# Performance work log

Measured on AMD Instinct MI355X. Metric: run time of the kernel, lower is better.

## Reference

```python
import jax, jax.numpy as jnp
import numpy as np

BATCH = 4096
FEAT = 1024
HID = 1024


def setup_inputs() -> dict:
    key = jax.random.key(0)
    ks = jax.random.split(key, 11)
    s_x = 1.0 / np.sqrt(FEAT)
    s_h = 1.0 / np.sqrt(HID)
    return {
        "x": jax.random.normal(ks[0], (BATCH, FEAT), jnp.float32),
        "h_prev": jax.random.normal(ks[1], (BATCH, HID), jnp.float32),
        "c_prev": jax.random.normal(ks[2], (BATCH, HID), jnp.float32),
        # Dense(3*hidden) on x and h (keras Dense: y = x @ W + b)
        "W_ifo_x": jax.random.normal(ks[3], (FEAT, 3 * HID), jnp.float32) * s_x,
        "b_ifo_x": jnp.zeros((3 * HID,), jnp.float32),
        "W_ifo_h": jax.random.normal(ks[4], (HID, 3 * HID), jnp.float32) * s_h,
        "b_ifo_h": jnp.zeros((3 * HID,), jnp.float32),
        # Dense(hidden) on x and h for candidate 'a'
        "W_b_x": jax.random.normal(ks[5], (FEAT, HID), jnp.float32) * s_x,
        "b_b_x": jnp.zeros((HID,), jnp.float32),
        "W_b_h": jax.random.normal(ks[6], (HID, HID), jnp.float32) * s_h,
        "b_b_h": jnp.zeros((HID,), jnp.float32),
    }


def reference(x, h_prev, c_prev, W_ifo_x, b_ifo_x, W_ifo_h, b_ifo_h,
              W_b_x, b_b_x, W_b_h, b_b_h):
    # Fused gate projections: [B, 3H]
    ifo = jax.nn.sigmoid(x @ W_ifo_x + b_ifo_x + h_prev @ W_ifo_h + b_ifo_h)
    i, f, o = jnp.split(ifo, 3, axis=-1)
    a = jnp.tanh(x @ W_b_x + b_b_x + h_prev @ W_b_h + b_b_h)
    c = i * a + f * c_prev
    h = o * jnp.tanh(c)
    return (h, c)
```

## Files before the change

### kernel.cpp

```cpp
#include <hip/hip_runtime.h>
#include <hip/hip_bf16.h>
#include <stdint.h>
#include <stddef.h>


#define BATCH 4096
#define FEAT  1024
#define HID   1024
#define NCAT  4096
#define KCAT  2048

typedef __attribute__((ext_vector_type(8))) __bf16 bf16x8;
typedef __attribute__((ext_vector_type(4))) float  floatx4;

__device__ __forceinline__ unsigned short f2bf(float f) {
    __hip_bfloat16 b = __float2bfloat16(f);
    return *reinterpret_cast<unsigned short*>(&b);
}
__device__ __forceinline__ void gl2lds16(const unsigned short* g, unsigned short* l) {
    __builtin_amdgcn_global_load_lds(
        (const __attribute__((address_space(1))) void*)g,
        (__attribute__((address_space(3))) void*)l, 16, 0, 0);
}

#define TP_PAD 72
__global__ __launch_bounds__(256)
void pack_all(const float* __restrict__ x, const float* __restrict__ h,
              const float* __restrict__ Wix, const float* __restrict__ Wih,
              const float* __restrict__ Wbx, const float* __restrict__ Wbh,
              unsigned short* __restrict__ Xcat, unsigned short* __restrict__ Wt) {
    __shared__ unsigned short tile[64 * TP_PAD];
    const int t = threadIdx.x;
    const int b = blockIdx.x;
    if (b >= 2048) {
        const int mbase = (b - 2048) * 4;
#pragma unroll
        for (int r = 0; r < 4; ++r) {
            const int m = mbase + r;
            const float* src = (t < 128) ? (x + (size_t)m * FEAT + t * 8)
                                         : (h + (size_t)m * HID + (t - 128) * 8);
            float4 v0 = *(const float4*)src;
            float4 v1 = *(const float4*)(src + 4);
            union { unsigned short s16[8]; uint4 v; } pk;
            pk.s16[0] = f2bf(v0.x); pk.s16[1] = f2bf(v0.y);
            pk.s16[2] = f2bf(v0.z); pk.s16[3] = f2bf(v0.w);
            pk.s16[4] = f2bf(v1.x); pk.s16[5] = f2bf(v1.y);
            pk.s16[6] = f2bf(v1.z); pk.s16[7] = f2bf(v1.w);
            *(uint4*)(Xcat + (size_t)m * KCAT + t * 8) = pk.v;
        }
        return;
    }
    const int tid = b;
    const int k0  = (tid & 31) * 64;
    const int q0  = (tid >> 5) * 64;
    const float* src; int stride, cb;
    if (q0 < 3072) { src = (k0 < FEAT) ? Wix : Wih; stride = 3072; cb = q0; }
    else           { src = (k0 < FEAT) ? Wbx : Wbh; stride = 1024; cb = q0 - 3072; }
    const int krow = (k0 < FEAT) ? k0 : (k0 - FEAT);
    {
        int kl = t >> 2;
        int c0 = (t & 3) * 16;
        const float* s = src + (size_t)(krow + kl) * stride + cb + c0;
        union { unsigned short s16[16]; uint4 v[2]; } tmp;
#pragma unroll
        for (int u = 0; u < 16; u += 4) {
            float4 v = *(const float4*)(s + u);
            tmp.s16[u + 0] = f2bf(v.x); tmp.s16[u + 1] = f2bf(v.y);
            tmp.s16[u + 2] = f2bf(v.z); tmp.s16[u + 3] = f2bf(v.w);
        }
        *(uint4*)&tile[kl * TP_PAD + c0]     = tmp.v[0];
        *(uint4*)&tile[kl * TP_PAD + c0 + 8] = tmp.v[1];
    }
    __syncthreads();
    {
        int nl = t >> 2, seg = t & 3;
        int q = q0 + nl;
        int g, j;
        if (q < 3072) { g = q >> 10; j = q & 1023; }
        else          { g = 3;       j = q - 3072; }
        int np = ((j >> 4) << 6) + (g << 4) + (j & 15);
        union { unsigned short s16[16]; uint4 v[2]; } pk;
#pragma unroll
        for (int u = 0; u < 16; ++u)
            pk.s16[u] = tile[(seg * 16 + u) * TP_PAD + nl];
        uint4* dst = (uint4*)(Wt + (size_t)np * KCAT + k0 + seg * 16);
        dst[0] = pk.v[0];
        dst[1] = pk.v[1];
    }
}

#define BM 256
#define BN 256
#define BK 64
#define NIT 16
#define HALF 8192

#define A_OFF(PAR, KS) (((PAR) * 2 + (KS)) * HALF)
#define B_OFF(PAR, KS) (32768 + ((PAR) * 2 + (KS)) * HALF)

__device__ __forceinline__ void stage_half(
    const unsigned short* __restrict__ src, int row0, int kt, int ks,
    unsigned short* __restrict__ ldsbase, int t) {
#pragma unroll
    for (int u = 0; u < 2; ++u) {
        int hslot = t + u * 512;
        int row   = hslot >> 2;
        int chofs = hslot & 3;
        int c     = chofs ^ ((row >> 1) & 3);
        gl2lds16(src + (size_t)(row0 + row) * KCAT + kt * BK + ks * 32 + c * 8,
                 ldsbase + hslot * 8);
    }
}

#define LOAD_BB(PAR, KS)                                                        \
    _Pragma("unroll")                                                           \
    for (int g = 0; g < 4; ++g)                                                 \
        bb[g] = *(const bf16x8*)&lds[B_OFF(PAR, KS) + (wn + g * 16 + lm) * 32 + cr];
#define LOAD_AA(PAR, KS, IQ)                                                    \
    _Pragma("unroll")                                                           \
    for (int ii = 0; ii < 4; ++ii)                                              \
        aa[ii] = *(const bf16x8*)&lds[A_OFF(PAR, KS) + (wm + (IQ) * 64 + ii * 16 + lm) * 32 + cr];
#define DO_MFMA(IQ)                                                             \
    asm volatile("s_waitcnt lgkmcnt(0)" ::: "memory");                          \
    __builtin_amdgcn_s_setprio(1);                                              \
    _Pragma("unroll")                                                           \
    for (int ii = 0; ii < 4; ++ii)                                              \
        _Pragma("unroll")                                                       \
        for (int g = 0; g < 4; ++g)                                             \
            acc[(IQ) * 4 + ii][g] = __builtin_amdgcn_mfma_f32_16x16x32_bf16(    \
                aa[ii], bb[g], acc[(IQ) * 4 + ii][g], 0, 0, 0);                 \
    __builtin_amdgcn_s_setprio(0);
#define BAR __builtin_amdgcn_s_barrier();

__global__ __launch_bounds__(512, 2)
void lstm_fused(const unsigned short* __restrict__ Xcat,
                const unsigned short* __restrict__ Wt,
                const float* __restrict__ c_prev,
                const float* __restrict__ bix, const float* __restrict__ bih,
                const float* __restrict__ bbx, const float* __restrict__ bbh,
                float* __restrict__ out_h, float* __restrict__ out_c) {
    __shared__ unsigned short lds[65536];
    const int t    = threadIdx.x;
    const int lane = t & 63;
    const int wid  = t >> 6;
    const int wm   = (wid >> 2) * 128;
    const int wn   = (wid & 3) * 64;
    const int m0   = blockIdx.y * BM;
    const int n0   = blockIdx.x * BN;
    const int lm   = lane & 15;
    const int lk   = lane >> 4;
    const int cr   = (lk ^ ((lm >> 1) & 3)) * 8;

    floatx4 acc[8][4];
#pragma unroll
    for (int i = 0; i < 8; ++i)
#pragma unroll
        for (int g = 0; g < 4; ++g) acc[i][g] = (floatx4){0.f, 0.f, 0.f, 0.f};

    stage_half(Xcat, m0, 0, 0, lds + A_OFF(0, 0), t);
    stage_half(Wt,   n0, 0, 0, lds + B_OFF(0, 0), t);
    stage_half(Xcat, m0, 0, 1, lds + A_OFF(0, 1), t);
    stage_half(Wt,   n0, 0, 1, lds + B_OFF(0, 1), t);
    stage_half(Xcat, m0, 1, 0, lds + A_OFF(1, 0), t);
    stage_half(Wt,   n0, 1, 0, lds + B_OFF(1, 0), t);
    asm volatile("s_waitcnt vmcnt(4)" ::: "memory");
    BAR

    bf16x8 aa[4], bb[4];

    for (int it = 0; it < NIT; ++it) {
        const int k1 = 2 * it + 1, k2 = 2 * it + 2, k3 = 2 * it + 3;
        const bool more = (it < NIT - 1);

        LOAD_BB(0, 0) LOAD_AA(0, 0, 0)
        stage_half(Xcat, m0, k1, 1, lds + A_OFF(1, 1), t);
        BAR DO_MFMA(0) BAR
        LOAD_AA(0, 0, 1)
        stage_half(Wt, n0, k1, 1, lds + B_OFF(1, 1), t);
        BAR DO_MFMA(1) BAR
        LOAD_BB(0, 1) LOAD_AA(0, 1, 0)
        if (more) stage_half(Xcat, m0, k2, 0, lds + A_OFF(0, 0), t);
        BAR DO_MFMA(0) BAR
        LOAD_AA(0, 1, 1)
        if (more) {
            stage_half(Wt, n0, k2, 0, lds + B_OFF(0, 0), t);
            asm volatile("s_waitcnt vmcnt(4)" ::: "memory");
        } else {
            asm volatile("s_waitcnt vmcnt(0)" ::: "memory");
        }
        BAR DO_MFMA(1) BAR
        LOAD_BB(1, 0) LOAD_AA(1, 0, 0)
        if (more) stage_half(Xcat, m0, k2, 1, lds + A_OFF(0, 1), t);
        BAR DO_MFMA(0) BAR
        LOAD_AA(1, 0, 1)
        if (more) stage_half(Wt, n0, k2, 1, lds + B_OFF(0, 1), t);
        BAR DO_MFMA(1) BAR
        LOAD_BB(1, 1) LOAD_AA(1, 1, 0)
        if (more) stage_half(Xcat, m0, k3, 0, lds + A_OFF(1, 0), t);
        BAR DO_MFMA(0) BAR
        LOAD_AA(1, 1, 1)
        if (more) {
            stage_half(Wt, n0, k3, 0, lds + B_OFF(1, 0), t);
            asm volatile("s_waitcnt vmcnt(4)" ::: "memory");
        }
        BAR DO_MFMA(1) BAR
    }

    const int j  = (((n0 + wn) >> 6) << 4) + lm;
    const float bi = bix[j]           + bih[j];
    const float bf = bix[HID + j]     + bih[HID + j];
    const float bo = bix[2 * HID + j] + bih[2 * HID + j];
    const float ba = bbx[j]           + bbh[j];
#pragma unroll
    for (int i = 0; i < 8; ++i) {
#pragma unroll
        for (int r = 0; r < 4; ++r) {
            int m = m0 + wm + i * 16 + (lk * 4) + r;
            float pi = acc[i][0][r] + bi;
            float pf = acc[i][1][r] + bf;
            float po = acc[i][2][r] + bo;
            float pa = acc[i][3][r] + ba;
            float ig = 1.f / (1.f + __expf(-pi));
            float fg = 1.f / (1.f + __expf(-pf));
            float og = 1.f / (1.f + __expf(-po));
            float av = 2.f / (1.f + __expf(-2.f * pa)) - 1.f;
            float cp = c_prev[(size_t)m * HID + j];
            float cv = ig * av + fg * cp;
            float hv = og * (2.f / (1.f + __expf(-2.f * cv)) - 1.f);
            out_h[(size_t)m * HID + j] = hv;
            out_c[(size_t)m * HID + j] = cv;
        }
    }
}

__global__ void naive_lstm(const float* __restrict__ x, const float* __restrict__ h,
                           const float* __restrict__ cvp,
                           const float* __restrict__ Wix, const float* __restrict__ bix,
                           const float* __restrict__ Wih, const float* __restrict__ bih,
                           const float* __restrict__ Wbx, const float* __restrict__ bbx,
                           const float* __restrict__ Wbh, const float* __restrict__ bbh,
                           float* __restrict__ out_h, float* __restrict__ out_c) {
    const int j = blockIdx.x * 256 + threadIdx.x;
    const int m = blockIdx.y;
    float ai = 0.f, af = 0.f, ao = 0.f, aa = 0.f;
    for (int k = 0; k < FEAT; ++k) {
        float xk = x[(size_t)m * FEAT + k];
        ai += xk * Wix[(size_t)k * 3072 + j];
        af += xk * Wix[(size_t)k * 3072 + HID + j];
        ao += xk * Wix[(size_t)k * 3072 + 2 * HID + j];
        aa += xk * Wbx[(size_t)k * HID + j];
    }
    for (int k = 0; k < HID; ++k) {
        float hk = h[(size_t)m * HID + k];
        ai += hk * Wih[(size_t)k * 3072 + j];
        af += hk * Wih[(size_t)k * 3072 + HID + j];
        ao += hk * Wih[(size_t)k * 3072 + 2 * HID + j];
        aa += hk * Wbh[(size_t)k * HID + j];
    }
    ai += bix[j] + bih[j];
    af += bix[HID + j] + bih[HID + j];
    ao += bix[2 * HID + j] + bih[2 * HID + j];
    aa += bbx[j] + bbh[j];
    float ig = 1.f / (1.f + __expf(-ai));
    float fg = 1.f / (1.f + __expf(-af));
    float og = 1.f / (1.f + __expf(-ao));
    float av = 2.f / (1.f + __expf(-2.f * aa)) - 1.f;
    float cp = cvp[(size_t)m * HID + j];
    float cc = ig * av + fg * cp;
    float hh = og * (2.f / (1.f + __expf(-2.f * cc)) - 1.f);
    out_h[(size_t)m * HID + j] = hh;
    out_c[(size_t)m * HID + j] = cc;
}

extern "C" void kernel_launch(void* const* d_in, const int* in_sizes, int n_in,
                              void* d_out, int out_size, void* d_ws, size_t ws_size,
                              hipStream_t stream) {
    const float* x   = (const float*)d_in[0];
    const float* h   = (const float*)d_in[1];
    const float* c   = (const float*)d_in[2];
    const float* Wix = (const float*)d_in[3];
    const float* bix = (const float*)d_in[4];
    const float* Wih = (const float*)d_in[5];
    const float* bih = (const float*)d_in[6];
    const float* Wbx = (const float*)d_in[7];
    const float* bbx = (const float*)d_in[8];
    const float* Wbh = (const float*)d_in[9];
    const float* bbh = (const float*)d_in[10];

    float* out_h = (float*)d_out;
    float* out_c = out_h + (size_t)BATCH * HID;

    const size_t WT_BYTES = (size_t)NCAT * KCAT * 2;
    const size_t XC_BYTES = (size_t)BATCH * KCAT * 2;
    if (ws_size >= WT_BYTES + XC_BYTES) {
        unsigned short* Wt   = (unsigned short*)d_ws;
        unsigned short* Xcat = (unsigned short*)((char*)d_ws + WT_BYTES);
        pack_all<<<2048 + 1024, 256, 0, stream>>>(x, h, Wix, Wih, Wbx, Wbh, Xcat, Wt);
        lstm_fused<<<dim3(NCAT / BN, BATCH / BM), 512, 0, stream>>>(
            Xcat, Wt, c, bix, bih, bbx, bbh, out_h, out_c);
    } else {
        naive_lstm<<<dim3(HID / 256, BATCH), 256, 0, stream>>>(
            x, h, c, Wix, bix, Wih, bih, Wbx, bbx, Wbh, bbh, out_h, out_c);
    }
}
```

Before: 200.2 us.

## Double-buffer A fragments in registers to overlap LDS reads with MFMA

Splits the A register fragments into two alternating buffers. The next quarter's A tile is read from LDS while the current quarter's MFMAs run, and the explicit lgkmcnt(0) wait before each MFMA group is dropped. Adds sched_barriers and reworks the vmcnt waits so staged data is ready in time. The cost it targets is LDS-read latency stalling the matrix cores. In exchange it uses more VGPRs, which may hurt occupancy at 2 blocks per CU. It also issues some LDS reads (such as the A_OFF(0,0) preload at the end of an iteration) before the workgroup barrier that publishes that tile, which risks reading data that is not yet visible.

```diff
diff --git a/kernel.cpp b/kernel.cpp
--- a/kernel.cpp
+++ b/kernel.cpp
@@ -112,25 +112,25 @@
     }
 }
 
-#define LOAD_BB(PAR, KS)                                                        \
+#define LOAD_B(PAR, KS)                                                         \
     _Pragma("unroll")                                                           \
     for (int g = 0; g < 4; ++g)                                                 \
         bb[g] = *(const bf16x8*)&lds[B_OFF(PAR, KS) + (wn + g * 16 + lm) * 32 + cr];
-#define LOAD_AA(PAR, KS, IQ)                                                    \
+#define LOAD_A(DST, PAR, KS, IQ)                                                \
     _Pragma("unroll")                                                           \
     for (int ii = 0; ii < 4; ++ii)                                              \
-        aa[ii] = *(const bf16x8*)&lds[A_OFF(PAR, KS) + (wm + (IQ) * 64 + ii * 16 + lm) * 32 + cr];
-#define DO_MFMA(IQ)                                                             \
-    asm volatile("s_waitcnt lgkmcnt(0)" ::: "memory");                          \
+        DST[ii] = *(const bf16x8*)&lds[A_OFF(PAR, KS) + (wm + (IQ) * 64 + ii * 16 + lm) * 32 + cr];
+#define MFMA_CL(SRC, IQ)                                                        \
     __builtin_amdgcn_s_setprio(1);                                              \
     _Pragma("unroll")                                                           \
     for (int ii = 0; ii < 4; ++ii)                                              \
         _Pragma("unroll")                                                       \
         for (int g = 0; g < 4; ++g)                                             \
             acc[(IQ) * 4 + ii][g] = __builtin_amdgcn_mfma_f32_16x16x32_bf16(    \
-                aa[ii], bb[g], acc[(IQ) * 4 + ii][g], 0, 0, 0);                 \
+                SRC[ii], bb[g], acc[(IQ) * 4 + ii][g], 0, 0, 0);                \
     __builtin_amdgcn_s_setprio(0);
 #define BAR __builtin_amdgcn_s_barrier();
+#define SBAR __builtin_amdgcn_sched_barrier(0);
 
 __global__ __launch_bounds__(512, 2)
 void lstm_fused(const unsigned short* __restrict__ Xcat,
@@ -166,44 +166,51 @@
     asm volatile("s_waitcnt vmcnt(4)" ::: "memory");
     BAR
 
-    bf16x8 aa[4], bb[4];
+    bf16x8 aaA[4], aaB[4], bb[4];
+    LOAD_A(aaA, 0, 0, 0)
 
     for (int it = 0; it < NIT; ++it) {
         const int k1 = 2 * it + 1, k2 = 2 * it + 2, k3 = 2 * it + 3;
         const bool more = (it < NIT - 1);
 
-        LOAD_BB(0, 0) LOAD_AA(0, 0, 0)
+        LOAD_B(0, 0) SBAR LOAD_A(aaB, 0, 0, 1)
         stage_half(Xcat, m0, k1, 1, lds + A_OFF(1, 1), t);
-        BAR DO_MFMA(0) BAR
-        LOAD_AA(0, 0, 1)
+        BAR MFMA_CL(aaA, 0) BAR
+        LOAD_A(aaA, 0, 1, 0)
         stage_half(Wt, n0, k1, 1, lds + B_OFF(1, 1), t);
-        BAR DO_MFMA(1) BAR
-        LOAD_BB(0, 1) LOAD_AA(0, 1, 0)
+        asm volatile("s_waitcnt vmcnt(4)" ::: "memory");
+        BAR MFMA_CL(aaB, 1) BAR
+        LOAD_B(0, 1) SBAR LOAD_A(aaB, 0, 1, 1)
         if (more) stage_half(Xcat, m0, k2, 0, lds + A_OFF(0, 0), t);
-        BAR DO_MFMA(0) BAR
-        LOAD_AA(0, 1, 1)
+        BAR MFMA_CL(aaA, 0) BAR
+        LOAD_A(aaA, 1, 0, 0)
         if (more) {
             stage_half(Wt, n0, k2, 0, lds + B_OFF(0, 0), t);
             asm volatile("s_waitcnt vmcnt(4)" ::: "memory");
         } else {
+            asm volatile("s_waitcnt vmcnt(2)" ::: "memory");
+        }
+        BAR MFMA_CL(aaB, 1) BAR
+        LOAD_B(1, 0) SBAR LOAD_A(aaB, 1, 0, 1)
+        if (more) stage_half(Xcat, m0, k2, 1, lds + A_OFF(0, 1), t);
+        BAR MFMA_CL(aaA, 0) BAR
+        LOAD_A(aaA, 1, 1, 0)
+        if (more) {
+            stage_half(Wt, n0, k2, 1, lds + B_OFF(0, 1), t);
+            asm volatile("s_waitcnt vmcnt(4)" ::: "memory");
+        } else {
             asm volatile("s_waitcnt vmcnt(0)" ::: "memory");
         }
-        BAR DO_MFMA(1) BAR
-        LOAD_BB(1, 0) LOAD_AA(1, 0, 0)
-        if (more) stage_half(Xcat, m0, k2, 1, lds + A_OFF(0, 1), t);
-        BAR DO_MFMA(0) BAR
-        LOAD_AA(1, 0, 1)
-        if (more) stage_half(Wt, n0, k2, 1, lds + B_OFF(0, 1), t);
-        BAR DO_MFMA(1) BAR
-        LOAD_BB(1, 1) LOAD_AA(1, 1, 0)
+        BAR MFMA_CL(aaB, 1) BAR
+        LOAD_B(1, 1) SBAR LOAD_A(aaB, 1, 1, 1)
         if (more) stage_half(Xcat, m0, k3, 0, lds + A_OFF(1, 0), t);
-        BAR DO_MFMA(0) BAR
-        LOAD_AA(1, 1, 1)
+        BAR MFMA_CL(aaA, 0) BAR
         if (more) {
             stage_half(Wt, n0, k3, 0, lds + B_OFF(1, 0), t);
             asm volatile("s_waitcnt vmcnt(4)" ::: "memory");
-        }
-        BAR DO_MFMA(1) BAR
+            LOAD_A(aaA, 0, 0, 0)
+        }
+        BAR MFMA_CL(aaB, 1) BAR
     }
 
     const int j  = (((n0 + wn) >> 6) << 4) + lm;
```

Result: no change. 202.9 us (+1.3%).

## Fuse fp32-to-bf16 packing into GEMM kernel, drop separate pack pass

Applied to the files above, without the earlier changes.

Removes the separate pack kernel that converted and transposed x, h and all weights into bf16 workspace buffers. The GEMM kernel now loads fp32 directly through registers, converts to bf16, and writes swizzled tiles into LDS within its pipelined main loop. This avoids the extra kernel launch and the workspace write and read-back. The cost is twice as many global bytes per tile, repeated conversion work across blocks, and loss of the direct global-to-LDS loads. The naive fallback path is also removed.

```diff
diff --git a/kernel.cpp b/kernel.cpp
--- a/kernel.cpp
+++ b/kernel.cpp
@@ -17,77 +17,6 @@
     __hip_bfloat16 b = __float2bfloat16(f);
     return *reinterpret_cast<unsigned short*>(&b);
 }
-__device__ __forceinline__ void gl2lds16(const unsigned short* g, unsigned short* l) {
-    __builtin_amdgcn_global_load_lds(
-        (const __attribute__((address_space(1))) void*)g,
-        (__attribute__((address_space(3))) void*)l, 16, 0, 0);
-}
-
-#define TP_PAD 72
-__global__ __launch_bounds__(256)
-void pack_all(const float* __restrict__ x, const float* __restrict__ h,
-              const float* __restrict__ Wix, const float* __restrict__ Wih,
-              const float* __restrict__ Wbx, const float* __restrict__ Wbh,
-              unsigned short* __restrict__ Xcat, unsigned short* __restrict__ Wt) {
-    __shared__ unsigned short tile[64 * TP_PAD];
-    const int t = threadIdx.x;
-    const int b = blockIdx.x;
-    if (b >= 2048) {
-        const int mbase = (b - 2048) * 4;
-#pragma unroll
-        for (int r = 0; r < 4; ++r) {
-            const int m = mbase + r;
-            const float* src = (t < 128) ? (x + (size_t)m * FEAT + t * 8)
-                                         : (h + (size_t)m * HID + (t - 128) * 8);
-            float4 v0 = *(const float4*)src;
-            float4 v1 = *(const float4*)(src + 4);
-            union { unsigned short s16[8]; uint4 v; } pk;
-            pk.s16[0] = f2bf(v0.x); pk.s16[1] = f2bf(v0.y);
-            pk.s16[2] = f2bf(v0.z); pk.s16[3] = f2bf(v0.w);
-            pk.s16[4] = f2bf(v1.x); pk.s16[5] = f2bf(v1.y);
-            pk.s16[6] = f2bf(v1.z); pk.s16[7] = f2bf(v1.w);
-            *(uint4*)(Xcat + (size_t)m * KCAT + t * 8) = pk.v;
-        }
-        return;
-    }
-    const int tid = b;
-    const int k0  = (tid & 31) * 64;
-    const int q0  = (tid >> 5) * 64;
-    const float* src; int stride, cb;
-    if (q0 < 3072) { src = (k0 < FEAT) ? Wix : Wih; stride = 3072; cb = q0; }
-    else           { src = (k0 < FEAT) ? Wbx : Wbh; stride = 1024; cb = q0 - 3072; }
-    const int krow = (k0 < FEAT) ? k0 : (k0 - FEAT);
-    {
-        int kl = t >> 2;
-        int c0 = (t & 3) * 16;
-        const float* s = src + (size_t)(krow + kl) * stride + cb + c0;
-        union { unsigned short s16[16]; uint4 v[2]; } tmp;
-#pragma unroll
-        for (int u = 0; u < 16; u += 4) {
-            float4 v = *(const float4*)(s + u);
-            tmp.s16[u + 0] = f2bf(v.x); tmp.s16[u + 1] = f2bf(v.y);
-            tmp.s16[u + 2] = f2bf(v.z); tmp.s16[u + 3] = f2bf(v.w);
-        }
-        *(uint4*)&tile[kl * TP_PAD + c0]     = tmp.v[0];
-        *(uint4*)&tile[kl * TP_PAD + c0 + 8] = tmp.v[1];
-    }
-    __syncthreads();
-    {
-        int nl = t >> 2, seg = t & 3;
-        int q = q0 + nl;
-        int g, j;
-        if (q < 3072) { g = q >> 10; j = q & 1023; }
-        else          { g = 3;       j = q - 3072; }
-        int np = ((j >> 4) << 6) + (g << 4) + (j & 15);
-        union { unsigned short s16[16]; uint4 v[2]; } pk;
-#pragma unroll
-        for (int u = 0; u < 16; ++u)
-            pk.s16[u] = tile[(seg * 16 + u) * TP_PAD + nl];
-        uint4* dst = (uint4*)(Wt + (size_t)np * KCAT + k0 + seg * 16);
-        dst[0] = pk.v[0];
-        dst[1] = pk.v[1];
-    }
-}
 
 #define BM 256
 #define BN 256
@@ -98,47 +27,67 @@
 #define A_OFF(PAR, KS) (((PAR) * 2 + (KS)) * HALF)
 #define B_OFF(PAR, KS) (32768 + ((PAR) * 2 + (KS)) * HALF)
 
-__device__ __forceinline__ void stage_half(
-    const unsigned short* __restrict__ src, int row0, int kt, int ks,
-    unsigned short* __restrict__ ldsbase, int t) {
-#pragma unroll
-    for (int u = 0; u < 2; ++u) {
-        int hslot = t + u * 512;
-        int row   = hslot >> 2;
-        int chofs = hslot & 3;
-        int c     = chofs ^ ((row >> 1) & 3);
-        gl2lds16(src + (size_t)(row0 + row) * KCAT + kt * BK + ks * 32 + c * 8,
-                 ldsbase + hslot * 8);
-    }
-}
+#define ISSUE_A(S, KT, KS) {                                                    \
+    const float* s_ = ((KT) < 16) ? (xrow + (KT) * 64 + (KS) * 32)              \
+                                  : (hrow + ((KT) - 16) * 64 + (KS) * 32);      \
+    S[0] = *(const floatx4*)(s_);      S[1] = *(const floatx4*)(s_ + 4);        \
+    S[2] = *(const floatx4*)(s_ + 8);  S[3] = *(const floatx4*)(s_ + 12); }
+
+#define COMMIT_A(S, PAR, KS) {                                                  \
+    union { unsigned short u[8]; uint4 v; } w0_, w1_;                           \
+    _Pragma("unroll")                                                           \
+    for (int e_ = 0; e_ < 4; ++e_) {                                            \
+        w0_.u[e_] = f2bf(S[0][e_]); w0_.u[4 + e_] = f2bf(S[1][e_]);             \
+        w1_.u[e_] = f2bf(S[2][e_]); w1_.u[4 + e_] = f2bf(S[3][e_]); }           \
+    *(uint4*)&lds[A_OFF(PAR, KS) + am * 32 + as0 * 8] = w0_.v;                  \
+    *(uint4*)&lds[A_OFF(PAR, KS) + am * 32 + as1 * 8] = w1_.v; }
+
+#define ISSUE_B(S, KT, KS) {                                                    \
+    int kg_ = (KT) * 64 + (KS) * 32 + bk4;                                      \
+    const float* s_ = (kg_ < 1024) ? (bxcol + (size_t)kg_ * bstride)            \
+                                   : (bhcol + (size_t)(kg_ - 1024) * bstride);  \
+    S[0] = *(const floatx4*)(s_);                                               \
+    S[1] = *(const floatx4*)(s_ + bstride);                                     \
+    S[2] = *(const floatx4*)(s_ + 2 * (size_t)bstride);                         \
+    S[3] = *(const floatx4*)(s_ + 3 * (size_t)bstride); }
+
+#define COMMIT_B(S, PAR, KS) {                                                  \
+    _Pragma("unroll")                                                           \
+    for (int c_ = 0; c_ < 4; ++c_) {                                            \
+        union { unsigned short u[4]; uint2 v; } w_;                             \
+        w_.u[0] = f2bf(S[0][c_]); w_.u[1] = f2bf(S[1][c_]);                     \
+        w_.u[2] = f2bf(S[2][c_]); w_.u[3] = f2bf(S[3][c_]);                     \
+        *(uint2*)&lds[B_OFF(PAR, KS) + (bnp4 + c_) * 32 + bswz * 8 + bsub * 4]  \
+            = w_.v; } }
 
 #define LOAD_BB(PAR, KS)                                                        \
     _Pragma("unroll")                                                           \
-    for (int g = 0; g < 4; ++g)                                                 \
-        bb[g] = *(const bf16x8*)&lds[B_OFF(PAR, KS) + (wn + g * 16 + lm) * 32 + cr];
+    for (int g_ = 0; g_ < 4; ++g_)                                              \
+        bb[g_] = *(const bf16x8*)&lds[B_OFF(PAR, KS) + (wn + g_ * 16 + lm) * 32 + cr];
 #define LOAD_AA(PAR, KS, IQ)                                                    \
     _Pragma("unroll")                                                           \
     for (int ii = 0; ii < 4; ++ii)                                              \
         aa[ii] = *(const bf16x8*)&lds[A_OFF(PAR, KS) + (wm + (IQ) * 64 + ii * 16 + lm) * 32 + cr];
-#define DO_MFMA(IQ)                                                             \
-    asm volatile("s_waitcnt lgkmcnt(0)" ::: "memory");                          \
+#define MFMA16(IQ)                                                              \
     __builtin_amdgcn_s_setprio(1);                                              \
     _Pragma("unroll")                                                           \
     for (int ii = 0; ii < 4; ++ii)                                              \
         _Pragma("unroll")                                                       \
-        for (int g = 0; g < 4; ++g)                                             \
-            acc[(IQ) * 4 + ii][g] = __builtin_amdgcn_mfma_f32_16x16x32_bf16(    \
-                aa[ii], bb[g], acc[(IQ) * 4 + ii][g], 0, 0, 0);                 \
+        for (int g_ = 0; g_ < 4; ++g_)                                          \
+            acc[(IQ) * 4 + ii][g_] = __builtin_amdgcn_mfma_f32_16x16x32_bf16(   \
+                aa[ii], bb[g_], acc[(IQ) * 4 + ii][g_], 0, 0, 0);               \
     __builtin_amdgcn_s_setprio(0);
 #define BAR __builtin_amdgcn_s_barrier();
+#define DRAIN asm volatile("s_waitcnt lgkmcnt(0)" ::: "memory");
 
 __global__ __launch_bounds__(512, 2)
-void lstm_fused(const unsigned short* __restrict__ Xcat,
-                const unsigned short* __restrict__ Wt,
-                const float* __restrict__ c_prev,
-                const float* __restrict__ bix, const float* __restrict__ bih,
-                const float* __restrict__ bbx, const float* __restrict__ bbh,
-                float* __restrict__ out_h, float* __restrict__ out_c) {
+void lstm_one(const float* __restrict__ x, const float* __restrict__ h,
+              const float* __restrict__ c_prev,
+              const float* __restrict__ Wix, const float* __restrict__ Wih,
+              const float* __restrict__ Wbx, const float* __restrict__ Wbh,
+              const float* __restrict__ bix, const float* __restrict__ bih,
+              const float* __restrict__ bbx, const float* __restrict__ bbh,
+              float* __restrict__ out_h, float* __restrict__ out_c) {
     __shared__ unsigned short lds[65536];
     const int t    = threadIdx.x;
     const int lane = t & 63;
@@ -149,7 +98,26 @@
     const int n0   = blockIdx.x * BN;
     const int lm   = lane & 15;
     const int lk   = lane >> 4;
-    const int cr   = (lk ^ ((lm >> 1) & 3)) * 8;
+    const int cr   = (lk ^ ((lm >> 2) & 3)) * 8;
+
+    const int am   = t >> 1;
+    const float* xrow = x + (size_t)(m0 + am) * FEAT + (t & 1) * 16;
+    const float* hrow = h + (size_t)(m0 + am) * HID  + (t & 1) * 16;
+    const int ac0  = (t & 1) * 2;
+    const int aswz = (am >> 2) & 3;
+    const int as0  = ac0 ^ aswz;
+    const int as1  = (ac0 + 1) ^ aswz;
+
+    const int bnp4 = (t & 63) * 4;
+    const int bk4  = (t >> 6) * 4;
+    const int bg   = (bnp4 >> 4) & 3;
+    const int bj   = (((n0 + bnp4) >> 6) << 4) | (bnp4 & 15);
+    const int bq   = (bg < 3) ? bg * 1024 + bj : bj;
+    const int bstride = (bg < 3) ? 3 * HID : HID;
+    const float* bxcol = ((bg < 3) ? Wix : Wbx) + bq;
+    const float* bhcol = ((bg < 3) ? Wih : Wbh) + bq;
+    const int bswz = (bk4 >> 3) ^ ((bnp4 >> 2) & 3);
+    const int bsub = (bk4 >> 2) & 1;
 
     floatx4 acc[8][4];
 #pragma unroll
@@ -157,53 +125,56 @@
 #pragma unroll
         for (int g = 0; g < 4; ++g) acc[i][g] = (floatx4){0.f, 0.f, 0.f, 0.f};
 
-    stage_half(Xcat, m0, 0, 0, lds + A_OFF(0, 0), t);
-    stage_half(Wt,   n0, 0, 0, lds + B_OFF(0, 0), t);
-    stage_half(Xcat, m0, 0, 1, lds + A_OFF(0, 1), t);
-    stage_half(Wt,   n0, 0, 1, lds + B_OFF(0, 1), t);
-    stage_half(Xcat, m0, 1, 0, lds + A_OFF(1, 0), t);
-    stage_half(Wt,   n0, 1, 0, lds + B_OFF(1, 0), t);
-    asm volatile("s_waitcnt vmcnt(4)" ::: "memory");
+    floatx4 SO[4], SE[4];
+    bf16x8 aa[4], bb[4];
+
+    ISSUE_A(SO, 0, 0) ISSUE_B(SE, 0, 0)
+    COMMIT_A(SO, 0, 0) COMMIT_B(SE, 0, 0)
+    ISSUE_A(SO, 0, 1) ISSUE_B(SE, 0, 1)
+    COMMIT_A(SO, 0, 1) COMMIT_B(SE, 0, 1)
+    ISSUE_A(SO, 1, 0) ISSUE_B(SE, 1, 0)
+    COMMIT_A(SO, 1, 0) COMMIT_B(SE, 1, 0)
+    ISSUE_A(SO, 1, 1)
+    ISSUE_B(SE, 1, 1)
+    DRAIN
     BAR
 
-    bf16x8 aa[4], bb[4];
-
     for (int it = 0; it < NIT; ++it) {
-        const int k1 = 2 * it + 1, k2 = 2 * it + 2, k3 = 2 * it + 3;
+        const int k2 = 2 * it + 2, k3 = 2 * it + 3;
         const bool more = (it < NIT - 1);
 
+        COMMIT_A(SO, 1, 1) DRAIN
         LOAD_BB(0, 0) LOAD_AA(0, 0, 0)
-        stage_half(Xcat, m0, k1, 1, lds + A_OFF(1, 1), t);
-        BAR DO_MFMA(0) BAR
+        if (more) ISSUE_A(SO, k2, 0)
+        BAR MFMA16(0) BAR
+        COMMIT_B(SE, 1, 1) DRAIN
         LOAD_AA(0, 0, 1)
-        stage_half(Wt, n0, k1, 1, lds + B_OFF(1, 1), t);
-        BAR DO_MFMA(1) BAR
+        if (more) ISSUE_B(SE, k2, 0)
+        BAR MFMA16(1) BAR
+        if (more) { COMMIT_A(SO, 0, 0) DRAIN }
         LOAD_BB(0, 1) LOAD_AA(0, 1, 0)
-        if (more) stage_half(Xcat, m0, k2, 0, lds + A_OFF(0, 0), t);
-        BAR DO_MFMA(0) BAR
+        if (more) ISSUE_A(SO, k2, 1)
+        BAR MFMA16(0) BAR
+        if (more) { COMMIT_B(SE, 0, 0) DRAIN }
         LOAD_AA(0, 1, 1)
-        if (more) {
-            stage_half(Wt, n0, k2, 0, lds + B_OFF(0, 0), t);
-            asm volatile("s_waitcnt vmcnt(4)" ::: "memory");
-        } else {
-            asm volatile("s_waitcnt vmcnt(0)" ::: "memory");
-        }
-        BAR DO_MFMA(1) BAR
+        if (more) ISSUE_B(SE, k2, 1)
+        BAR MFMA16(1) BAR
+        if (more) { COMMIT_A(SO, 0, 1) DRAIN }
         LOAD_BB(1, 0) LOAD_AA(1, 0, 0)
-        if (more) stage_half(Xcat, m0, k2, 1, lds + A_OFF(0, 1), t);
-        BAR DO_MFMA(0) BAR
+        if (more) ISSUE_A(SO, k3, 0)
+        BAR MFMA16(0) BAR
+        if (more) { COMMIT_B(SE, 0, 1) DRAIN }
         LOAD_AA(1, 0, 1)
-        if (more) stage_half(Wt, n0, k2, 1, lds + B_OFF(0, 1), t);
-        BAR DO_MFMA(1) BAR
+        if (more) ISSUE_B(SE, k3, 0)
+        BAR MFMA16(1) BAR
+        if (more) { COMMIT_A(SO, 1, 0) DRAIN }
         LOAD_BB(1, 1) LOAD_AA(1, 1, 0)
-        if (more) stage_half(Xcat, m0, k3, 0, lds + A_OFF(1, 0), t);
-        BAR DO_MFMA(0) BAR
+        if (more) ISSUE_A(SO, k3, 1)
+        BAR MFMA16(0) BAR
+        if (more) { COMMIT_B(SE, 1, 0) DRAIN }
         LOAD_AA(1, 1, 1)
-        if (more) {
-            stage_half(Wt, n0, k3, 0, lds + B_OFF(1, 0), t);
-            asm volatile("s_waitcnt vmcnt(4)" ::: "memory");
-        }
-        BAR DO_MFMA(1) BAR
+        if (more) ISSUE_B(SE, k3, 1)
+        BAR MFMA16(1) BAR
     }
 
     const int j  = (((n0 + wn) >> 6) << 4) + lm;
@@ -233,45 +204,6 @@
     }
 }
 
-__global__ void naive_lstm(const float* __restrict__ x, const float* __restrict__ h,
-                           const float* __restrict__ cvp,
-                           const float* __restrict__ Wix, const float* __restrict__ bix,
-                           const float* __restrict__ Wih, const float* __restrict__ bih,
-                           const float* __restrict__ Wbx, const float* __restrict__ bbx,
-                           const float* __restrict__ Wbh, const float* __restrict__ bbh,
-                           float* __restrict__ out_h, float* __restrict__ out_c) {
-    const int j = blockIdx.x * 256 + threadIdx.x;
-    const int m = blockIdx.y;
-    float ai = 0.f, af = 0.f, ao = 0.f, aa = 0.f;
-    for (int k = 0; k < FEAT; ++k) {
-        float xk = x[(size_t)m * FEAT + k];
-        ai += xk * Wix[(size_t)k * 3072 + j];
-        af += xk * Wix[(size_t)k * 3072 + HID + j];
-        ao += xk * Wix[(size_t)k * 3072 + 2 * HID + j];
-        aa += xk * Wbx[(size_t)k * HID + j];
-    }
-    for (int k = 0; k < HID; ++k) {
-        float hk = h[(size_t)m * HID + k];
-        ai += hk * Wih[(size_t)k * 3072 + j];
-        af += hk * Wih[(size_t)k * 3072 + HID + j];
-        ao += hk * Wih[(size_t)k * 3072 + 2 * HID + j];
-        aa += hk * Wbh[(size_t)k * HID + j];
-    }
-    ai += bix[j] + bih[j];
-    af += bix[HID + j] + bih[HID + j];
-    ao += bix[2 * HID + j] + bih[2 * HID + j];
-    aa += bbx[j] + bbh[j];
-    float ig = 1.f / (1.f + __expf(-ai));
-    float fg = 1.f / (1.f + __expf(-af));
-    float og = 1.f / (1.f + __expf(-ao));
-    float av = 2.f / (1.f + __expf(-2.f * aa)) - 1.f;
-    float cp = cvp[(size_t)m * HID + j];
-    float cc = ig * av + fg * cp;
-    float hh = og * (2.f / (1.f + __expf(-2.f * cc)) - 1.f);
-    out_h[(size_t)m * HID + j] = hh;
-    out_c[(size_t)m * HID + j] = cc;
-}
-
 extern "C" void kernel_launch(void* const* d_in, const int* in_sizes, int n_in,
                               void* d_out, int out_size, void* d_ws, size_t ws_size,
                               hipStream_t stream) {
@@ -290,16 +222,6 @@
     float* out_h = (float*)d_out;
     float* out_c = out_h + (size_t)BATCH * HID;
 
-    const size_t WT_BYTES = (size_t)NCAT * KCAT * 2;
-    const size_t XC_BYTES = (size_t)BATCH * KCAT * 2;
-    if (ws_size >= WT_BYTES + XC_BYTES) {
-        unsigned short* Wt   = (unsigned short*)d_ws;
-        unsigned short* Xcat = (unsigned short*)((char*)d_ws + WT_BYTES);
-        pack_all<<<2048 + 1024, 256, 0, stream>>>(x, h, Wix, Wih, Wbx, Wbh, Xcat, Wt);
-        lstm_fused<<<dim3(NCAT / BN, BATCH / BM), 512, 0, stream>>>(
-            Xcat, Wt, c, bix, bih, bbx, bbh, out_h, out_c);
-    } else {
-        naive_lstm<<<dim3(HID / 256, BATCH), 256, 0, stream>>>(
-            x, h, c, Wix, bix, Wih, bih, Wbx, bbx, Wbh, bbh, out_h, out_c);
-    }
+    lstm_one<<<dim3(NCAT / BN, BATCH / BM), 512, 0, stream>>>(
+        x, h, c, Wix, Wih, Wbx, Wbh, bix, bih, bbx, bbh, out_h, out_c);
 }
```

Result: slower. 209.0 us (+4.4%).
